# Performance work log

Measured on AMD Instinct MI355X. Metric: run time of the kernel, lower is better.

Reference implementation:

```python
import jax, jax.numpy as jnp
import numpy as np


def setup_inputs() -> dict:
    key = jax.random.key(0)
    k1, k2 = jax.random.split(key)
    inputs = jax.random.normal(k1, (4, 128, 64, 64), dtype=jnp.float32)
    # binary hole mask (1 = known background, 0 = hole), broadcast over channels
    mask = jnp.round(jax.random.uniform(k2, (4, 1, 64, 64), dtype=jnp.float32))
    return {"inputs": inputs, "mask": mask}


def reference(inputs, mask):
    # SFFA contextual attention with 1x1 dynamic kernels.
    # Note: in the original torch code the 1x1 conv with padding=1 produces
    # border scores that conv_transpose2d with padding=1 crops away exactly,
    # so the math reduces to per-pixel matmul + softmax + matmul.
    bz, nc, h, w = inputs.shape
    N = h * w
    background = inputs * mask                              # [b, c, h, w]
    # dynamic kernels: one nc-dim vector per background pixel (patch)
    K = background.reshape(bz, nc, N).transpose(0, 2, 1) + 1e-7   # [b, N, c]
    Kn = K / jnp.sqrt(jnp.sum(K * K, axis=2, keepdims=True))      # l2-normalized
    feat = inputs.reshape(bz, nc, N)                        # [b, c, N]
    scores = jnp.einsum('bpc,bcn->bpn', Kn, feat)           # [b, N(patch), N(pixel)]
    attn = jax.nn.softmax(scores, axis=1)                   # softmax over patches p
    agg = jnp.einsum('bpc,bpn->bcn', K, attn).reshape(bz, nc, h, w)
    return background + agg * (1.0 - mask)
```

## Files before the change

### kernel.cpp

```cpp
#include <hip/hip_runtime.h>
#include <hip/hip_bf16.h>

typedef __attribute__((ext_vector_type(8))) short bf16x8;
typedef __attribute__((ext_vector_type(4))) float f32x4;

#define NPIX 4096
#define NC   128
#define RS128 0.08838834764831845f

__global__ __launch_bounds__(1024) void sffa_prep(
    const float* __restrict__ x, const float* __restrict__ mask,
    ushort* __restrict__ KnW, ushort* __restrict__ QW, ushort* __restrict__ VtW,
    float* __restrict__ s0c, int* __restrict__ pixQ, int* __restrict__ cnts,
    float* __restrict__ out)
{
    __shared__ float xs[128][69];
    __shared__ float ms[64];
    __shared__ float rinv[64];
    __shared__ float ssum[64];
    __shared__ float2 part[16][64];
    __shared__ int se[64];
    __shared__ int bgn[64];
    __shared__ int tinfo[2];
    __shared__ int wredP[16], wredT[16];
    const int tid = threadIdx.x;
    const int b = blockIdx.x >> 6, nblk = blockIdx.x & 63;
    const int n0 = nblk * 64;
    const float* xb = x + (size_t)b * NC * NPIX;
    float* ob = out + (size_t)b * NC * NPIX;

    #pragma unroll
    for (int it = 0; it < 2; ++it) {
        int e4 = it * 1024 + tid;
        int c = e4 >> 4, n4 = (e4 & 15) * 4;
        float4 v = *(const float4*)(xb + (size_t)c * NPIX + n0 + n4);
        xs[c][n4+0] = v.x; xs[c][n4+1] = v.y; xs[c][n4+2] = v.z; xs[c][n4+3] = v.w;
        *(float4*)(ob + (size_t)c * NPIX + n0 + n4) = v;
    }
    if (tid < 16) {
        float4 mv = *(const float4*)(mask + (size_t)b * NPIX + n0 + tid * 4);
        ms[tid*4+0] = mv.x; ms[tid*4+1] = mv.y; ms[tid*4+2] = mv.z; ms[tid*4+3] = mv.w;
    }
    {
        const int lane = tid & 63, w = tid >> 6;
        float4 mv = *(const float4*)(mask + (size_t)b * NPIX + tid * 4);
        int f0 = mv.x < 0.5f ? 0x10000 : 1;
        int f1 = mv.y < 0.5f ? 0x10000 : 1;
        int f2 = mv.z < 0.5f ? 0x10000 : 1;
        int f3 = mv.w < 0.5f ? 0x10000 : 1;
        int p0 = tid * 4;
        int pre = 0, tot = f0 + f1 + f2 + f3;
        if (p0 + 0 < n0) pre += f0;
        if (p0 + 1 < n0) pre += f1;
        if (p0 + 2 < n0) pre += f2;
        if (p0 + 3 < n0) pre += f3;
        #pragma unroll
        for (int d = 1; d < 64; d <<= 1) {
            pre += __shfl_xor(pre, d);
            tot += __shfl_xor(tot, d);
        }
        if (lane == 0) { wredP[w] = pre; wredT[w] = tot; }
    }
    __syncthreads();
    if (tid < 64) {
        int vP = (tid < 16) ? wredP[tid] : 0;
        int vT = (tid < 16) ? wredT[tid] : 0;
        #pragma unroll
        for (int d = 1; d < 16; d <<= 1) {
            vP += __shfl_xor(vP, d);
            vT += __shfl_xor(vT, d);
        }
        int base  = __shfl(vP, 0);
        int total = __shfl(vT, 0);
        if (tid == 0 && nblk == 0) {
            cnts[b * 2]     = total & 0xffff;
            cnts[b * 2 + 1] = total >> 16;
        }
        int f = ms[tid] > 0.5f ? 1 : 0x10000;
        int s = f;
        #pragma unroll
        for (int d = 1; d < 64; d <<= 1) {
            int t = __shfl_up(s, d);
            if (tid >= d) s += t;
        }
        se[tid] = base + s - f;
    }
    __syncthreads();
    {
        int p = tid & 63, qd = tid >> 6;
        float m = ms[p];
        float s2 = 0.f, s1 = 0.f;
        #pragma unroll
        for (int i = 0; i < 8; ++i) {
            float xv = xs[qd*8 + i][p];
            float k = fmaf(xv, m, 1e-7f);
            s2 = fmaf(k, k, s2);
            s1 += xv;
        }
        part[qd][p] = make_float2(s2, s1);
    }
    __syncthreads();
    if (tid < 64) {
        float s2 = 0.f, s1 = 0.f;
        #pragma unroll
        for (int k = 0; k < 16; ++k) { float2 t = part[k][tid]; s2 += t.x; s1 += t.y; }
        rinv[tid] = rsqrtf(s2);
        ssum[tid] = s1 * RS128;
    }
    __syncthreads();
    #pragma unroll
    for (int it = 0; it < 4; ++it) {
        int e2 = it * 1024 + tid;
        int n = e2 >> 6, cp = (e2 & 63) * 2;
        int pe = se[n];
        float x0 = xs[cp][n], x1 = xs[cp+1][n];
        if (ms[n] > 0.5f) {
            int slot = pe & 0xffff;
            float k0 = x0 + 1e-7f, k1 = x1 + 1e-7f;
            float r = rinv[n];
            __hip_bfloat162 kn;
            kn.x = __float2bfloat16(k0 * r); kn.y = __float2bfloat16(k1 * r);
            *(__hip_bfloat162*)(KnW + ((size_t)b * NPIX + slot) * NC + cp) = kn;
        } else {
            int slot = pe >> 16;
            __hip_bfloat162 q;
            q.x = __float2bfloat16(x0); q.y = __float2bfloat16(x1);
            *(__hip_bfloat162*)(QW + ((size_t)b * NPIX + slot) * NC + cp) = q;
        }
    }
    if (tid < 64) {
        if (ms[tid] < 0.5f) {
            int slot = se[tid] >> 16;
            s0c [(size_t)b * NPIX + slot] = ssum[tid];
            pixQ[(size_t)b * NPIX + slot] = n0 + tid;
        } else {
            bgn[(se[tid] & 0xffff) - (se[0] & 0xffff)] = tid;
        }
    }
    if (tid == 0) {
        tinfo[0] = se[0] & 0xffff;
        tinfo[1] = (se[63] & 0xffff) + (ms[63] > 0.5f ? 1 : 0) - (se[0] & 0xffff);
    }
    __syncthreads();
    {
        const int s0b = tinfo[0], nbg = tinfo[1];
        const int j = tid & 63, cg = tid >> 6;
        if (j < nbg) {
            int n = bgn[j];
            ushort* vcol = VtW + (size_t)b * NC * NPIX + s0b + j;
            #pragma unroll
            for (int cc = 0; cc < 8; ++cc) {
                int c = cg * 8 + cc;
                __hip_bfloat16 h = __float2bfloat16(xs[c][n] + 1e-7f);
                vcol[(size_t)c * NPIX] = *(ushort*)&h;
            }
        }
    }
}

#define L_BUF 32768
#define L_P   65536
#define L_ML  75776
#define L_SCL 76800
#define L_PIX 77056
#define L_SZ  77312

__global__ __launch_bounds__(512, 2) void sffa_attn(
    const ushort* __restrict__ KnW, const ushort* __restrict__ QW,
    const ushort* __restrict__ VtW, const int* __restrict__ cnts,
    const float* __restrict__ s0c, const int* __restrict__ pixQ,
    float* __restrict__ out)
{
    __shared__ __align__(16) char smem[L_SZ];
    const int tid  = threadIdx.x;
    const int w = tid >> 6, lane = tid & 63;
    const int l15 = lane & 15, g = lane >> 4;
    const int bx = (int)blockIdx.x;
    const int b = bx >> 6, qblk = bx & 63;
    const int q0 = qblk * 64;
    const int cntK = cnts[b * 2], cntQ = cnts[b * 2 + 1];
    if (q0 >= cntQ) return;

    const int NTK = (cntK + 63) >> 6;
    float* ob = out + (size_t)b * NC * NPIX;

    if (NTK <= 0) {
        if (tid < 64) {
            int slot = q0 + tid;
            if (slot < cntQ) {
                int pix = pixQ[(size_t)b * NPIX + slot];
                for (int c = 0; c < NC; ++c) ob[(size_t)c * NPIX + pix] = 0.f;
            }
        }
        return;
    }

    const int half = w >> 2;
    const int wq   = w & 3;

    const ushort* Knb = KnW + (size_t)b * NPIX * NC;
    const ushort* Qb  = QW  + (size_t)b * NPIX * NC + (size_t)q0 * NC;
    const ushort* Vtb = VtW + (size_t)b * NC * NPIX;

    #pragma unroll
    for (int it = 0; it < 2; ++it) {
        int L = (it * 512 + tid) * 16;
        int row = L >> 8, col = L & 255;
        int4 v = *(const int4*)((const char*)Qb + L);
        *(int4*)(smem + row * 256 + (col ^ ((row & 15) << 4))) = v;
    }
    __syncthreads();
    bf16x8 qf[4];
    {
        int qrow = wq * 16 + l15;
        #pragma unroll
        for (int kc = 0; kc < 4; ++kc)
            qf[kc] = *(const bf16x8*)(smem + qrow * 256 + ((64*kc + 16*g) ^ (l15 << 4)));
    }
    __syncthreads();

    const int kOff = (tid >> 4) * 256 + (((tid & 15) * 16) ^ (((tid >> 4) & 15) << 4));
    const int cV = tid >> 3, sV = tid & 7;
    const int vOff = cV * 128 + ((sV * 16) ^ ((cV & 7) << 4));
    const int4* kgbase = (const int4*)Knb;
    const ushort* vgbase = Vtb + (size_t)cV * NPIX + sV * 8;

    int4 pr0, pr1, pr2, pr3;
    pr0 = kgbase[tid]; pr1 = kgbase[512 + tid];
    pr2 = *(const int4*)(vgbase);
    pr3 = *(const int4*)(vgbase + (size_t)64 * NPIX);
    {
        char* base = smem;
        *(int4*)(base + kOff) = pr0;
        *(int4*)(base + kOff + 8192) = pr1;
        *(int4*)(base + 16384 + vOff) = pr2;
        *(int4*)(base + 16384 + vOff + 8192) = pr3;
    }
    if (NTK > 1) {
        pr0 = kgbase[1024 + tid]; pr1 = kgbase[1536 + tid];
        pr2 = *(const int4*)(vgbase + 64);
        pr3 = *(const int4*)(vgbase + (size_t)64 * NPIX + 64);
    }
    __syncthreads();

    f32x4 acc[8];
    const f32x4 fzero = {0.f, 0.f, 0.f, 0.f};
    #pragma unroll
    for (int i = 0; i < 8; ++i) acc[i] = fzero;
    float mrun = -1e30f, lrun = 0.f;
    char* Pw = smem + L_P + w * 1280;

    for (int kt = 0; kt < NTK; ++kt) {
        if (kt + 1 < NTK) {
            char* base = smem + ((kt + 1) & 1) * L_BUF;
            *(int4*)(base + kOff) = pr0;
            *(int4*)(base + kOff + 8192) = pr1;
            *(int4*)(base + 16384 + vOff) = pr2;
            *(int4*)(base + 16384 + vOff + 8192) = pr3;
        }
        if (kt + 2 < NTK) {
            pr0 = kgbase[(kt + 2) * 1024 + tid];
            pr1 = kgbase[(kt + 2) * 1024 + 512 + tid];
            pr2 = *(const int4*)(vgbase + (kt + 2) * 64);
            pr3 = *(const int4*)(vgbase + (size_t)64 * NPIX + (kt + 2) * 64);
        }
        char* bb = smem + (kt & 1) * L_BUF;
        f32x4 sa0 = fzero, sa1 = fzero;
        {
            const char* rb0 = bb + (half * 32 + l15) * 256;
            const char* rb1 = rb0 + 4096;
            const int sw = l15 << 4;
            __builtin_amdgcn_s_setprio(1);
            #pragma unroll
            for (int kc = 0; kc < 4; ++kc) {
                int off = (64 * kc + 16 * g) ^ sw;
                bf16x8 a0 = *(const bf16x8*)(rb0 + off);
                bf16x8 a1 = *(const bf16x8*)(rb1 + off);
                sa0 = __builtin_amdgcn_mfma_f32_16x16x32_bf16(a0, qf[kc], sa0, 0, 0, 0);
                sa1 = __builtin_amdgcn_mfma_f32_16x16x32_bf16(a1, qf[kc], sa1, 0, 0, 0);
            }
            __builtin_amdgcn_s_setprio(0);
        }
        {
            int kg0 = kt * 64;
            if (kg0 + 64 > cntK) {
                int kb = cntK - kg0;
                int kr = half * 32 + 4 * g;
                #pragma unroll
                for (int r = 0; r < 4; ++r) {
                    if (kr + r >= kb)      sa0[r] = -3e38f;
                    if (kr + 16 + r >= kb) sa1[r] = -3e38f;
                }
            }
        }
        float tmax = fmaxf(fmaxf(fmaxf(sa0[0], sa0[1]), fmaxf(sa0[2], sa0[3])),
                           fmaxf(fmaxf(sa1[0], sa1[1]), fmaxf(sa1[2], sa1[3])));
        tmax = fmaxf(tmax, __shfl_xor(tmax, 16));
        tmax = fmaxf(tmax, __shfl_xor(tmax, 32));
        bool grow = !__all(tmax <= mrun + 8.f);
        float mnew = grow ? fmaxf(mrun, tmax) : mrun;
        float p0[4], p1[4];
        float ts = 0.f;
        #pragma unroll
        for (int r = 0; r < 4; ++r) { p0[r] = __expf(sa0[r] - mnew); ts += p0[r]; }
        #pragma unroll
        for (int r = 0; r < 4; ++r) { p1[r] = __expf(sa1[r] - mnew); ts += p1[r]; }
        ts += __shfl_xor(ts, 16);
        ts += __shfl_xor(ts, 32);
        if (grow) {
            float sc = __expf(mrun - mnew);
            lrun = lrun * sc + ts;
            float scr[4];
            #pragma unroll
            for (int r = 0; r < 4; ++r) scr[r] = __shfl(sc, 4 * g + r);
            #pragma unroll
            for (int ct = 0; ct < 8; ++ct) {
                acc[ct][0] *= scr[0]; acc[ct][1] *= scr[1];
                acc[ct][2] *= scr[2]; acc[ct][3] *= scr[3];
            }
            mrun = mnew;
        } else {
            lrun += ts;
        }
        union { __hip_bfloat162 h; unsigned u; } ua0, ua1, ub0, ub1;
        ua0.h.x = __float2bfloat16(p0[0]); ua0.h.y = __float2bfloat16(p0[1]);
        ua1.h.x = __float2bfloat16(p0[2]); ua1.h.y = __float2bfloat16(p0[3]);
        ub0.h.x = __float2bfloat16(p1[0]); ub0.h.y = __float2bfloat16(p1[1]);
        ub1.h.x = __float2bfloat16(p1[2]); ub1.h.y = __float2bfloat16(p1[3]);
        *(int2*)(Pw + l15 * 80 +      8 * g) = make_int2((int)ua0.u, (int)ua1.u);
        *(int2*)(Pw + l15 * 80 + 32 + 8 * g) = make_int2((int)ub0.u, (int)ub1.u);
        bf16x8 pf = *(const bf16x8*)(Pw + l15 * 80 + 16 * g);
        {
            const char* vb = bb + 16384;
            __builtin_amdgcn_s_setprio(1);
            #pragma unroll
            for (int ct = 0; ct < 8; ++ct) {
                int c = 16 * ct + l15;
                bf16x8 vf = *(const bf16x8*)(vb + c * 128 +
                                             ((64 * half + 16 * g) ^ ((c & 7) << 4)));
                acc[ct] = __builtin_amdgcn_mfma_f32_16x16x32_bf16(pf, vf, acc[ct], 0, 0, 0);
            }
            __builtin_amdgcn_s_setprio(0);
        }
        __syncthreads();
    }

    float* ma = (float*)(smem + L_ML);
    float* la = ma + 64; float* mb = la + 64; float* lb = mb + 64;
    const int q = wq * 16 + l15;
    if (g == 0) {
        if (half == 0) { ma[q] = mrun; la[q] = lrun; }
        else           { mb[q] = mrun; lb[q] = lrun; }
    }
    __syncthreads();
    float* agg = (float*)smem;
    {
        float mstar = fmaxf(ma[q], mb[q]);
        float f = __expf(mrun - mstar);
        float fr[4];
        #pragma unroll
        for (int r = 0; r < 4; ++r) fr[r] = __shfl(f, 4 * g + r);
        if (half == 1) {
            #pragma unroll
            for (int ct = 0; ct < 8; ++ct) {
                int c = 16 * ct + l15;
                #pragma unroll
                for (int r = 0; r < 4; ++r)
                    agg[c * 68 + wq * 16 + 4 * g + r] = acc[ct][r] * fr[r];
            }
        }
        __syncthreads();
        if (half == 0) {
            #pragma unroll
            for (int ct = 0; ct < 8; ++ct) {
                int c = 16 * ct + l15;
                #pragma unroll
                for (int r = 0; r < 4; ++r) {
                    int idx = c * 68 + wq * 16 + 4 * g + r;
                    agg[idx] = acc[ct][r] * fr[r] + agg[idx];
                }
            }
        }
    }
    __syncthreads();

    float* scl  = (float*)(smem + L_SCL);
    int*   pixS = (int*)(smem + L_PIX);
    const float m0f = (float)(NPIX - cntK);
    if (tid < 64) {
        int slot = q0 + tid;
        int pix = -1;
        float sv = 0.f;
        if (slot < cntQ) {
            pix = pixQ[(size_t)b * NPIX + slot];
            float M  = fmaxf(ma[tid], mb[tid]);
            float ls = la[tid] * __expf(ma[tid] - M) + lb[tid] * __expf(mb[tid] - M);
            float s0 = s0c[(size_t)b * NPIX + slot];
            float M2 = fmaxf(M, s0);
            float eM = __expf(M - M2);
            float L  = m0f * __expf(s0 - M2) + ls * eM;
            sv = eM / L;
        }
        scl[tid]  = sv;
        pixS[tid] = pix;
    }
    __syncthreads();
    #pragma unroll
    for (int it = 0; it < 2; ++it) {
        int idx = it * 512 + tid;
        int c = idx >> 3, grp = idx & 7;
        #pragma unroll
        for (int j = 0; j < 8; ++j) {
            int sq = grp * 8 + j;
            int pix = pixS[sq];
            if (pix >= 0)
                ob[(size_t)c * NPIX + pix] = agg[c * 68 + sq] * scl[sq];
        }
    }
}

extern "C" void kernel_launch(void* const* d_in, const int* in_sizes, int n_in,
                              void* d_out, int out_size, void* d_ws, size_t ws_size,
                              hipStream_t stream) {
    const float* x    = (const float*)d_in[0];
    const float* mask = (const float*)d_in[1];
    char* ws = (char*)d_ws;
    const size_t MBy = 1024 * 1024;
    const size_t KBy = 1024;

    ushort* KnW = (ushort*)(ws);
    ushort* QW  = (ushort*)(ws + 4 * MBy);
    ushort* VtW = (ushort*)(ws + 8 * MBy);
    char* tail = ws + 12 * MBy;
    float* s0c  = (float*)(tail);
    int*   pixQ = (int*)(tail + 64 * KBy);
    int*   cnts = (int*)(tail + 128 * KBy);

    sffa_prep <<<256, 1024, 0, stream>>>(x, mask, KnW, QW, VtW, s0c, pixQ, cnts,
                                         (float*)d_out);
    sffa_attn <<<256, 512, 0, stream>>>(KnW, QW, VtW, cnts, s0c, pixQ,
                                        (float*)d_out);
}
```

Before: 56.84 us.

## Halve query tile, double key tile, split keys four ways across waves

The attention kernel now processes 32 queries per block instead of 64 and launches twice as many blocks. Each block loads 128-key K/V tiles, which are double-buffered in LDS. The eight waves are arranged as 2 query groups by 4 key quarters, and the partial softmax/accumulator results are merged through LDS in four serialized passes. The goal is to fill more CUs when only about half the pixels are holes, at the cost of ~140KB LDS per block (one block per CU), more redundant K/V loading across blocks and extra reduction synchronisation.

```diff
diff --git a/kernel.cpp b/kernel.cpp
--- a/kernel.cpp
+++ b/kernel.cpp
@@ -158,12 +158,12 @@
     }
 }
 
-#define L_BUF 32768
-#define L_P   65536
-#define L_ML  75776
-#define L_SCL 76800
-#define L_PIX 77056
-#define L_SZ  77312
+#define L_BUFSZ 65536
+#define L_P   131072
+#define L_ML  141312
+#define L_SCL 142336
+#define L_PIX 142464
+#define L_SZ  142592
 
 __global__ __launch_bounds__(512, 2) void sffa_attn(
     const ushort* __restrict__ KnW, const ushort* __restrict__ QW,
@@ -176,16 +176,16 @@
     const int w = tid >> 6, lane = tid & 63;
     const int l15 = lane & 15, g = lane >> 4;
     const int bx = (int)blockIdx.x;
-    const int b = bx >> 6, qblk = bx & 63;
-    const int q0 = qblk * 64;
+    const int b = bx >> 7, qblk = bx & 127;
+    const int q0 = qblk * 32;
     const int cntK = cnts[b * 2], cntQ = cnts[b * 2 + 1];
     if (q0 >= cntQ) return;
 
-    const int NTK = (cntK + 63) >> 6;
+    const int NTK = (cntK + 127) >> 7;
     float* ob = out + (size_t)b * NC * NPIX;
 
     if (NTK <= 0) {
-        if (tid < 64) {
+        if (tid < 32) {
             int slot = q0 + tid;
             if (slot < cntQ) {
                 int pix = pixQ[(size_t)b * NPIX + slot];
@@ -195,18 +195,16 @@
         return;
     }
 
-    const int half = w >> 2;
-    const int wq   = w & 3;
+    const int wq = w & 1;
+    const int kq = w >> 1;
 
     const ushort* Knb = KnW + (size_t)b * NPIX * NC;
     const ushort* Qb  = QW  + (size_t)b * NPIX * NC + (size_t)q0 * NC;
     const ushort* Vtb = VtW + (size_t)b * NC * NPIX;
 
-    #pragma unroll
-    for (int it = 0; it < 2; ++it) {
-        int L = (it * 512 + tid) * 16;
-        int row = L >> 8, col = L & 255;
-        int4 v = *(const int4*)((const char*)Qb + L);
+    {
+        int row = tid >> 4, col = (tid & 15) * 16;
+        int4 v = ((const int4*)Qb)[tid];
         *(int4*)(smem + row * 256 + (col ^ ((row & 15) << 4))) = v;
     }
     __syncthreads();
@@ -219,27 +217,35 @@
     }
     __syncthreads();
 
-    const int kOff = (tid >> 4) * 256 + (((tid & 15) * 16) ^ (((tid >> 4) & 15) << 4));
-    const int cV = tid >> 3, sV = tid & 7;
-    const int vOff = cV * 128 + ((sV * 16) ^ ((cV & 7) << 4));
+    const int sOff = (tid >> 4) * 256 + (((tid & 15) * 16) ^ (((tid >> 4) & 15) << 4));
     const int4* kgbase = (const int4*)Knb;
-    const ushort* vgbase = Vtb + (size_t)cV * NPIX + sV * 8;
-
-    int4 pr0, pr1, pr2, pr3;
-    pr0 = kgbase[tid]; pr1 = kgbase[512 + tid];
-    pr2 = *(const int4*)(vgbase);
-    pr3 = *(const int4*)(vgbase + (size_t)64 * NPIX);
-    {
-        char* base = smem;
-        *(int4*)(base + kOff) = pr0;
-        *(int4*)(base + kOff + 8192) = pr1;
-        *(int4*)(base + 16384 + vOff) = pr2;
-        *(int4*)(base + 16384 + vOff + 8192) = pr3;
+    const ushort* vg = Vtb + (size_t)(tid >> 4) * NPIX + (tid & 15) * 8;
+
+    int4 prK0, prK1, prK2, prK3, prV0, prV1, prV2, prV3;
+    prK0 = kgbase[tid];        prK1 = kgbase[512 + tid];
+    prK2 = kgbase[1024 + tid]; prK3 = kgbase[1536 + tid];
+    prV0 = *(const int4*)(vg);
+    prV1 = *(const int4*)(vg + (size_t)32 * NPIX);
+    prV2 = *(const int4*)(vg + (size_t)64 * NPIX);
+    prV3 = *(const int4*)(vg + (size_t)96 * NPIX);
+    {
+        char* bk = smem, * bv = smem + 32768;
+        *(int4*)(bk + sOff)         = prK0;
+        *(int4*)(bk + sOff + 8192)  = prK1;
+        *(int4*)(bk + sOff + 16384) = prK2;
+        *(int4*)(bk + sOff + 24576) = prK3;
+        *(int4*)(bv + sOff)         = prV0;
+        *(int4*)(bv + sOff + 8192)  = prV1;
+        *(int4*)(bv + sOff + 16384) = prV2;
+        *(int4*)(bv + sOff + 24576) = prV3;
     }
     if (NTK > 1) {
-        pr0 = kgbase[1024 + tid]; pr1 = kgbase[1536 + tid];
-        pr2 = *(const int4*)(vgbase + 64);
-        pr3 = *(const int4*)(vgbase + (size_t)64 * NPIX + 64);
+        prK0 = kgbase[2048 + tid];  prK1 = kgbase[2560 + tid];
+        prK2 = kgbase[3072 + tid];  prK3 = kgbase[3584 + tid];
+        prV0 = *(const int4*)(vg + 128);
+        prV1 = *(const int4*)(vg + (size_t)32 * NPIX + 128);
+        prV2 = *(const int4*)(vg + (size_t)64 * NPIX + 128);
+        prV3 = *(const int4*)(vg + (size_t)96 * NPIX + 128);
     }
     __syncthreads();
 
@@ -252,22 +258,32 @@
 
     for (int kt = 0; kt < NTK; ++kt) {
         if (kt + 1 < NTK) {
-            char* base = smem + ((kt + 1) & 1) * L_BUF;
-            *(int4*)(base + kOff) = pr0;
-            *(int4*)(base + kOff + 8192) = pr1;
-            *(int4*)(base + 16384 + vOff) = pr2;
-            *(int4*)(base + 16384 + vOff + 8192) = pr3;
+            char* bk = smem + ((kt + 1) & 1) * L_BUFSZ;
+            char* bv = bk + 32768;
+            *(int4*)(bk + sOff)         = prK0;
+            *(int4*)(bk + sOff + 8192)  = prK1;
+            *(int4*)(bk + sOff + 16384) = prK2;
+            *(int4*)(bk + sOff + 24576) = prK3;
+            *(int4*)(bv + sOff)         = prV0;
+            *(int4*)(bv + sOff + 8192)  = prV1;
+            *(int4*)(bv + sOff + 16384) = prV2;
+            *(int4*)(bv + sOff + 24576) = prV3;
         }
         if (kt + 2 < NTK) {
-            pr0 = kgbase[(kt + 2) * 1024 + tid];
-            pr1 = kgbase[(kt + 2) * 1024 + 512 + tid];
-            pr2 = *(const int4*)(vgbase + (kt + 2) * 64);
-            pr3 = *(const int4*)(vgbase + (size_t)64 * NPIX + (kt + 2) * 64);
-        }
-        char* bb = smem + (kt & 1) * L_BUF;
+            int kb4 = (kt + 2) * 2048;
+            prK0 = kgbase[kb4 + tid];        prK1 = kgbase[kb4 + 512 + tid];
+            prK2 = kgbase[kb4 + 1024 + tid]; prK3 = kgbase[kb4 + 1536 + tid];
+            const ushort* vgk = vg + (kt + 2) * 128;
+            prV0 = *(const int4*)(vgk);
+            prV1 = *(const int4*)(vgk + (size_t)32 * NPIX);
+            prV2 = *(const int4*)(vgk + (size_t)64 * NPIX);
+            prV3 = *(const int4*)(vgk + (size_t)96 * NPIX);
+        }
+        char* bk = smem + (kt & 1) * L_BUFSZ;
+        char* bv = bk + 32768;
         f32x4 sa0 = fzero, sa1 = fzero;
         {
-            const char* rb0 = bb + (half * 32 + l15) * 256;
+            const char* rb0 = bk + (kq * 32 + l15) * 256;
             const char* rb1 = rb0 + 4096;
             const int sw = l15 << 4;
             __builtin_amdgcn_s_setprio(1);
@@ -282,10 +298,10 @@
             __builtin_amdgcn_s_setprio(0);
         }
         {
-            int kg0 = kt * 64;
-            if (kg0 + 64 > cntK) {
+            int kg0 = kt * 128;
+            if (kg0 + 128 > cntK) {
                 int kb = cntK - kg0;
-                int kr = half * 32 + 4 * g;
+                int kr = kq * 32 + 4 * g;
                 #pragma unroll
                 for (int r = 0; r < 4; ++r) {
                     if (kr + r >= kb)      sa0[r] = -3e38f;
@@ -331,13 +347,12 @@
         *(int2*)(Pw + l15 * 80 + 32 + 8 * g) = make_int2((int)ub0.u, (int)ub1.u);
         bf16x8 pf = *(const bf16x8*)(Pw + l15 * 80 + 16 * g);
         {
-            const char* vb = bb + 16384;
             __builtin_amdgcn_s_setprio(1);
             #pragma unroll
             for (int ct = 0; ct < 8; ++ct) {
                 int c = 16 * ct + l15;
-                bf16x8 vf = *(const bf16x8*)(vb + c * 128 +
-                                             ((64 * half + 16 * g) ^ ((c & 7) << 4)));
+                bf16x8 vf = *(const bf16x8*)(bv + c * 256 +
+                                             ((64 * kq + 16 * g) ^ ((c & 15) << 4)));
                 acc[ct] = __builtin_amdgcn_mfma_f32_16x16x32_bf16(pf, vf, acc[ct], 0, 0, 0);
             }
             __builtin_amdgcn_s_setprio(0);
@@ -346,55 +361,51 @@
     }
 
     float* ma = (float*)(smem + L_ML);
-    float* la = ma + 64; float* mb = la + 64; float* lb = mb + 64;
-    const int q = wq * 16 + l15;
-    if (g == 0) {
-        if (half == 0) { ma[q] = mrun; la[q] = lrun; }
-        else           { mb[q] = mrun; lb[q] = lrun; }
-    }
+    float* la = ma + 128;
+    const int qs = wq * 16 + l15;
+    if (g == 0) { ma[kq * 32 + qs] = mrun; la[kq * 32 + qs] = lrun; }
     __syncthreads();
     float* agg = (float*)smem;
     {
-        float mstar = fmaxf(ma[q], mb[q]);
+        float mstar = fmaxf(fmaxf(ma[qs], ma[32 + qs]), fmaxf(ma[64 + qs], ma[96 + qs]));
         float f = __expf(mrun - mstar);
         float fr[4];
         #pragma unroll
         for (int r = 0; r < 4; ++r) fr[r] = __shfl(f, 4 * g + r);
-        if (half == 1) {
-            #pragma unroll
-            for (int ct = 0; ct < 8; ++ct) {
-                int c = 16 * ct + l15;
+        #pragma unroll
+        for (int p = 0; p < 4; ++p) {
+            if (kq == p) {
                 #pragma unroll
-                for (int r = 0; r < 4; ++r)
-                    agg[c * 68 + wq * 16 + 4 * g + r] = acc[ct][r] * fr[r];
-            }
-        }
-        __syncthreads();
-        if (half == 0) {
-            #pragma unroll
-            for (int ct = 0; ct < 8; ++ct) {
-                int c = 16 * ct + l15;
-                #pragma unroll
-                for (int r = 0; r < 4; ++r) {
-                    int idx = c * 68 + wq * 16 + 4 * g + r;
-                    agg[idx] = acc[ct][r] * fr[r] + agg[idx];
+                for (int ct = 0; ct < 8; ++ct) {
+                    int c = 16 * ct + l15;
+                    #pragma unroll
+                    for (int r = 0; r < 4; ++r) {
+                        int idx = c * 36 + wq * 16 + 4 * g + r;
+                        float v = acc[ct][r] * fr[r];
+                        if (p == 0) agg[idx] = v;
+                        else        agg[idx] += v;
+                    }
                 }
             }
-        }
-    }
-    __syncthreads();
+            __syncthreads();
+        }
+    }
 
     float* scl  = (float*)(smem + L_SCL);
     int*   pixS = (int*)(smem + L_PIX);
     const float m0f = (float)(NPIX - cntK);
-    if (tid < 64) {
+    if (tid < 32) {
         int slot = q0 + tid;
         int pix = -1;
         float sv = 0.f;
         if (slot < cntQ) {
             pix = pixQ[(size_t)b * NPIX + slot];
-            float M  = fmaxf(ma[tid], mb[tid]);
-            float ls = la[tid] * __expf(ma[tid] - M) + lb[tid] * __expf(mb[tid] - M);
+            float M = fmaxf(fmaxf(ma[tid], ma[32 + tid]),
+                            fmaxf(ma[64 + tid], ma[96 + tid]));
+            float ls = la[tid]      * __expf(ma[tid]      - M)
+                     + la[32 + tid] * __expf(ma[32 + tid] - M)
+                     + la[64 + tid] * __expf(ma[64 + tid] - M)
+                     + la[96 + tid] * __expf(ma[96 + tid] - M);
             float s0 = s0c[(size_t)b * NPIX + slot];
             float M2 = fmaxf(M, s0);
             float eM = __expf(M - M2);
@@ -405,16 +416,14 @@
         pixS[tid] = pix;
     }
     __syncthreads();
-    #pragma unroll
-    for (int it = 0; it < 2; ++it) {
-        int idx = it * 512 + tid;
-        int c = idx >> 3, grp = idx & 7;
+    {
+        int c = tid >> 2, j0 = (tid & 3) * 8;
         #pragma unroll
         for (int j = 0; j < 8; ++j) {
-            int sq = grp * 8 + j;
-            int pix = pixS[sq];
+            int q = j0 + j;
+            int pix = pixS[q];
             if (pix >= 0)
-                ob[(size_t)c * NPIX + pix] = agg[c * 68 + sq] * scl[sq];
+                ob[(size_t)c * NPIX + pix] = agg[c * 36 + q] * scl[q];
         }
     }
 }
@@ -438,6 +447,6 @@
 
     sffa_prep <<<256, 1024, 0, stream>>>(x, mask, KnW, QW, VtW, s0c, pixQ, cnts,
                                          (float*)d_out);
-    sffa_attn <<<256, 512, 0, stream>>>(KnW, QW, VtW, cnts, s0c, pixQ,
-                                        (float*)d_out);
+    sffa_attn <<<4 * 128, 512, 0, stream>>>(KnW, QW, VtW, cnts, s0c, pixQ,
+                                            (float*)d_out);
 }
```

Result: slower. 66.62 us (+17.2%).
